# Performance work log

Hardware: AMD Instinct MI355X
Metric: run time of the kernel (lower is better)

The kernel has to match this reference:

```python
import jax, jax.numpy as jnp
import numpy as np

B, N, E, H = 16, 577, 1024, 16          # batch, tokens (1 cls + 24x24 patches), embed, heads
HD = E // H
LORA_E, LORA_R = 4, 16                   # LoRA experts, rank
AD_E, AD_D = 4, 64                       # adapter experts, bottleneck
FF = 4 * E


def setup_inputs() -> dict:
    key = jax.random.key(0)
    ks = jax.random.split(key, 12)
    p = lambda i, shape: jax.random.normal(ks[i], shape, dtype=jnp.float32) * 0.02
    return {
        "tokens": jax.random.normal(ks[0], (B, N, E), dtype=jnp.float32),
        "ln1_g": jnp.ones((E,), jnp.float32), "ln1_b": jnp.zeros((E,), jnp.float32),
        "qkv_w": p(1, (3 * E, E)), "qkv_b": jnp.zeros((3 * E,), jnp.float32),
        "proj_w": p(2, (E, E)), "proj_b": jnp.zeros((E,), jnp.float32),
        "lora_gate_w": p(3, (LORA_E, E)),
        "lora_A": p(4, (LORA_E, LORA_R, E)),
        "lora_B": p(5, (LORA_E, 3 * E, LORA_R)),
        "ln2_g": jnp.ones((E,), jnp.float32), "ln2_b": jnp.zeros((E,), jnp.float32),
        "fc1_w": p(6, (FF, E)), "fc1_b": jnp.zeros((FF,), jnp.float32),
        "fc2_w": p(7, (E, FF)), "fc2_b": jnp.zeros((E,), jnp.float32),
        "ad_gate_w": p(8, (AD_E, E)),
        "ad_down_w": p(9, (AD_E, AD_D, E)), "ad_down_b": jnp.zeros((AD_E, AD_D), jnp.float32),
        "ad_up_w": p(10, (AD_E, E, AD_D)), "ad_up_b": jnp.zeros((AD_E, E), jnp.float32),
    }


def _ln(x, g, b):
    m = x.mean(-1, keepdims=True)
    v = ((x - m) ** 2).mean(-1, keepdims=True)
    return (x - m) * jax.lax.rsqrt(v + 1e-6) * g + b


def reference(tokens, ln1_g, ln1_b, qkv_w, qkv_b, proj_w, proj_b,
              lora_gate_w, lora_A, lora_B, ln2_g, ln2_b,
              fc1_w, fc1_b, fc2_w, fc2_b,
              ad_gate_w, ad_down_w, ad_down_b, ad_up_w, ad_up_b):
    # ---- attention with MoE-LoRA delta on fused QKV ----
    normed = _ln(tokens, ln1_g, ln1_b)                      # [B,N,E]
    qkv = normed @ qkv_w.T + qkv_b                          # [B,N,3E]
    gates = jax.nn.softmax(normed @ lora_gate_w.T, axis=-1)  # [B,N,X]
    h = jnp.einsum('bnd,xrd->bnxr', normed, lora_A)         # low-rank down
    delta = jnp.einsum('bnxr,bnx,xor->bno', h, gates, lora_B)  # gate-weighted up
    qkv = (qkv + delta).reshape(B, N, 3, H, HD).transpose(2, 0, 3, 1, 4)
    q, k, v = qkv[0], qkv[1], qkv[2]                        # [B,H,N,hd]
    scores = jnp.einsum('bhqd,bhkd->bhqk', q, k) * (HD ** -0.5)
    probs = jax.nn.softmax(scores, axis=-1)
    ctx = jnp.einsum('bhqk,bhkd->bhqd', probs, v)
    ctx = ctx.transpose(0, 2, 1, 3).reshape(B, N, E)
    tokens = tokens + (ctx @ proj_w.T + proj_b)
    # ---- MLP + MoE adapter branch (shared norm2 input) ----
    mlp_in = _ln(tokens, ln2_g, ln2_b)
    mlp_out = jax.nn.gelu(mlp_in @ fc1_w.T + fc1_b, approximate=False) @ fc2_w.T + fc2_b
    ag = jax.nn.softmax(mlp_in @ ad_gate_w.T, axis=-1)       # [B,N,Xa]
    ah = jax.nn.gelu(jnp.einsum('bnd,xhd->bnxh', mlp_in, ad_down_w) + ad_down_b,
                     approximate=False)
    ad_out = (jnp.einsum('bnxh,bnx,xoh->bno', ah, ag, ad_up_w)
              + jnp.einsum('bnx,xo->bno', ag, ad_up_b))
    return tokens + mlp_out + ad_out
```

## Files before the change

### kernel.cpp

```cpp
#include <hip/hip_runtime.h>
#include <math.h>

#define TOK 9232
#define EMB 1024
#define NQKV 3072
#define FFD 4096
#define NSEQ 577

typedef __bf16 bf16x8 __attribute__((ext_vector_type(8)));
typedef float f32x4 __attribute__((ext_vector_type(4)));
typedef unsigned short ushort8 __attribute__((ext_vector_type(8)));
typedef unsigned short ushort4v __attribute__((ext_vector_type(4)));

typedef __attribute__((address_space(3))) unsigned int lds_u32_t;
typedef const __attribute__((address_space(1))) unsigned int glob_u32_t;

__device__ __forceinline__ void async16(void* lds, const void* g) {
    __builtin_amdgcn_global_load_lds((glob_u32_t*)g, (lds_u32_t*)lds, 16, 0, 0);
}

__device__ __forceinline__ unsigned short f2bf(float f) {
    unsigned int u = __builtin_bit_cast(unsigned int, f);
    u = (u + 0x7fffu + ((u >> 16) & 1u)) >> 16;
    return (unsigned short)u;
}
__device__ __forceinline__ float bf2f(unsigned short s) {
    unsigned int u = ((unsigned int)s) << 16;
    return __builtin_bit_cast(float, u);
}
__device__ __forceinline__ float gelu_exact(float x) {
    return 0.5f * x * (1.0f + erff(x * 0.70710678118654752f));
}

__global__ void k_pack_all(const float* __restrict__ s_qkv, const float* __restrict__ s_proj,
                           const float* __restrict__ s_fc1, const float* __restrict__ s_fc2,
                           const float* __restrict__ s_la,  const float* __restrict__ s_ad,
                           unsigned short* __restrict__ d_qkv, unsigned short* __restrict__ d_proj,
                           unsigned short* __restrict__ d_fc1, unsigned short* __restrict__ d_fc2,
                           unsigned short* __restrict__ d_la,  unsigned short* __restrict__ d_ad) {
    int stride = gridDim.x * 256;
    for (int i4 = blockIdx.x * 256 + threadIdx.x; i4 < 3227648; i4 += stride) {
        const float* s; unsigned short* d; int local;
        if (i4 < 786432)       { s = s_qkv;  d = d_qkv;  local = i4; }
        else if (i4 < 1048576) { s = s_proj; d = d_proj; local = i4 - 786432; }
        else if (i4 < 2097152) { s = s_fc1;  d = d_fc1;  local = i4 - 1048576; }
        else if (i4 < 3145728) { s = s_fc2;  d = d_fc2;  local = i4 - 2097152; }
        else if (i4 < 3162112) { s = s_la;   d = d_la;   local = i4 - 3145728; }
        else                   { s = s_ad;   d = d_ad;   local = i4 - 3162112; }
        float4 v = ((const float4*)s)[local];
        ushort4v o;
        o[0] = f2bf(v.x); o[1] = f2bf(v.y); o[2] = f2bf(v.z); o[3] = f2bf(v.w);
        ((ushort4v*)d)[local] = o;
    }
}
__global__ void k_pack_bcat(const float* __restrict__ Bw, unsigned short* __restrict__ out) {
    int i = blockIdx.x * 256 + threadIdx.x;
    if (i >= 3072 * 64) return;
    int o = i >> 6, j = i & 63, x = j >> 4, r = j & 15;
    out[o * 64 + j] = f2bf(Bw[x * 3072 * 16 + o * 16 + r]);
}
__global__ void k_pack_u(const float* __restrict__ Uw, unsigned short* __restrict__ out) {
    int i = blockIdx.x * 256 + threadIdx.x;
    if (i >= 1024 * 256) return;
    int o = i >> 8, j = i & 255, x = j >> 6, h = j & 63;
    out[o * 256 + j] = f2bf(Uw[x * 65536 + o * 64 + h]);
}

__global__ __launch_bounds__(256) void k_ln_gates(const float* __restrict__ x,
                                                  const float* __restrict__ g,
                                                  const float* __restrict__ b,
                                                  const float* __restrict__ gw,
                                                  unsigned short* __restrict__ out,
                                                  float* __restrict__ gates) {
    int t = blockIdx.x;
    int tid = threadIdx.x;
    const float* xp = x + (size_t)t * EMB;
    float4 v = ((const float4*)xp)[tid];
    float s = v.x + v.y + v.z + v.w;
    float sq = v.x * v.x + v.y * v.y + v.z * v.z + v.w * v.w;
    #pragma unroll
    for (int off = 32; off > 0; off >>= 1) {
        s += __shfl_down(s, off);
        sq += __shfl_down(sq, off);
    }
    __shared__ float red[8];
    if ((tid & 63) == 0) { red[tid >> 6] = s; red[(tid >> 6) + 4] = sq; }
    __syncthreads();
    float S = red[0] + red[1] + red[2] + red[3];
    float SQ = red[4] + red[5] + red[6] + red[7];
    float mean = S * (1.0f / EMB);
    float var = SQ * (1.0f / EMB) - mean * mean;
    float rstd = rsqrtf(var + 1e-6f);
    float4 gv = ((const float4*)g)[tid];
    float4 bv = ((const float4*)b)[tid];
    float n0 = (v.x - mean) * rstd * gv.x + bv.x;
    float n1 = (v.y - mean) * rstd * gv.y + bv.y;
    float n2 = (v.z - mean) * rstd * gv.z + bv.z;
    float n3 = (v.w - mean) * rstd * gv.w + bv.w;
    ushort4v o;
    o[0] = f2bf(n0); o[1] = f2bf(n1); o[2] = f2bf(n2); o[3] = f2bf(n3);
    ((ushort4v*)(out + (size_t)t * EMB))[tid] = o;
    float p[4];
    #pragma unroll
    for (int xx = 0; xx < 4; ++xx) {
        float4 gr = ((const float4*)(gw + xx * EMB))[tid];
        p[xx] = n0 * gr.x + n1 * gr.y + n2 * gr.z + n3 * gr.w;
    }
    #pragma unroll
    for (int off = 32; off > 0; off >>= 1) {
        #pragma unroll
        for (int xx = 0; xx < 4; ++xx) p[xx] += __shfl_down(p[xx], off);
    }
    __shared__ float red2[4][4];
    if ((tid & 63) == 0) {
        #pragma unroll
        for (int xx = 0; xx < 4; ++xx) red2[tid >> 6][xx] = p[xx];
    }
    __syncthreads();
    if (tid == 0) {
        float l[4];
        #pragma unroll
        for (int xx = 0; xx < 4; ++xx) l[xx] = red2[0][xx] + red2[1][xx] + red2[2][xx] + red2[3][xx];
        float m = fmaxf(fmaxf(l[0], l[1]), fmaxf(l[2], l[3]));
        float e[4], ssum = 0.f;
        #pragma unroll
        for (int xx = 0; xx < 4; ++xx) { e[xx] = expf(l[xx] - m); ssum += e[xx]; }
        float inv = 1.0f / ssum;
        #pragma unroll
        for (int xx = 0; xx < 4; ++xx) gates[t * 4 + xx] = e[xx] * inv;
    }
}

__global__ __launch_bounds__(256) void k_fc2init(const float* __restrict__ tok2,
                                                 const float* __restrict__ fc2b,
                                                 const float* __restrict__ ag,
                                                 const float* __restrict__ upb,
                                                 float* __restrict__ out) {
    int t = blockIdx.x;
    int tid = threadIdx.x;
    float g0 = ag[t * 4 + 0], g1 = ag[t * 4 + 1], g2 = ag[t * 4 + 2], g3 = ag[t * 4 + 3];
    float4 b0 = ((const float4*)(upb + 0 * EMB))[tid];
    float4 b1 = ((const float4*)(upb + 1 * EMB))[tid];
    float4 b2 = ((const float4*)(upb + 2 * EMB))[tid];
    float4 b3 = ((const float4*)(upb + 3 * EMB))[tid];
    float4 fb = ((const float4*)fc2b)[tid];
    float4 r = ((const float4*)(tok2 + (size_t)t * EMB))[tid];
    r.x += fb.x + g0 * b0.x + g1 * b1.x + g2 * b2.x + g3 * b3.x;
    r.y += fb.y + g0 * b0.y + g1 * b1.y + g2 * b2.y + g3 * b3.y;
    r.z += fb.z + g0 * b0.z + g1 * b1.z + g2 * b2.z + g3 * b3.z;
    r.w += fb.w + g0 * b0.w + g1 * b1.w + g2 * b2.w + g3 * b3.w;
    ((float4*)(out + (size_t)t * EMB))[tid] = r;
}

#define BAR __builtin_amdgcn_s_barrier()

template<bool GELU, bool BF16OUT, int GG, int MF>
__global__ __launch_bounds__(256) void k_gemm(
    const unsigned short* __restrict__ A, int lda,
    const unsigned short* __restrict__ W, int ldw, int K1,
    int M, int N,
    const unsigned short* __restrict__ A2, const unsigned short* __restrict__ W2, int K2,
    const float* __restrict__ bias, const float* __restrict__ resid,
    const float* __restrict__ aux,
    void* __restrict__ Cout, int ldc, int gy)
{
    constexpr int CA = MF * 2;
    constexpr int CPW = (CA + 8) / 4;
    constexpr int BUFB = (CA + 8) * 1024;
    __shared__ __attribute__((aligned(16))) char Sbuf[3 * BUFB];

    int tid = threadIdx.x;
    int nwg = gridDim.x, orig = blockIdx.x;
    int xcd = orig & 7, lid = orig >> 3;
    int q = nwg >> 3, r = nwg & 7;
    int wg = (xcd < r ? xcd * (q + 1) : r * (q + 1) + (xcd - r) * q) + lid;
    int bm = (wg / gy) * (MF * 32);
    int bn = (wg % gy) * 128;

    int l = tid & 63, w = tid >> 6;
    int wr = w >> 1, wc = w & 1;
    int lr = l & 15;
    int sslot = (((l & 3) ^ ((l >> 3) & 3)) << 3);

    int KT1 = K1 >> 5, KT2 = K2 >> 5;
    int KT = KT1 + KT2;

    const unsigned short* A2s = A2 ? A2 : A;
    const unsigned short* W2s = W2 ? W2 : W;
    int K2s = A2 ? K2 : lda;

    const unsigned short* sp1[CPW];
    const unsigned short* sp2[CPW];
    int ldsu[CPW];
    #pragma unroll
    for (int j = 0; j < CPW; ++j) {
        int c = w * CPW + j;
        ldsu[j] = c << 10;
        if (c < CA) {
            int rw = bm + c * 16 + (l >> 2); if (rw > M - 1) rw = M - 1;
            sp1[j] = A + (size_t)rw * lda + sslot;
            sp2[j] = A2s + (size_t)rw * K2s + sslot;
        } else {
            int rw = bn + (c - CA) * 16 + (l >> 2); if (rw > N - 1) rw = N - 1;
            sp1[j] = W + (size_t)rw * ldw + sslot;
            sp2[j] = W2s + (size_t)rw * K2s + sslot;
        }
    }

    int psl = ((l >> 4) ^ ((lr >> 1) & 3)) << 4;
    int offA[MF], offB[4];
    #pragma unroll
    for (int m = 0; m < MF; ++m) offA[m] = ((wr * (MF * 16) + m * 16 + lr) << 6) + psl;
    #pragma unroll
    for (int n = 0; n < 4; ++n) offB[n] = (CA << 10) + ((wc * 64 + n * 16 + lr) << 6) + psl;

    f32x4 acc[MF][4];
    #pragma unroll
    for (int m = 0; m < MF; ++m)
        #pragma unroll
        for (int n = 0; n < 4; ++n) acc[m][n] = (f32x4){0.f, 0.f, 0.f, 0.f};

    auto stage = [&](int ss, int sb_) {
        char* db = Sbuf + sb_ * BUFB;
        if (ss < KT1) {
            int ko = ss << 5;
            #pragma unroll
            for (int j = 0; j < CPW; ++j) async16(db + ldsu[j], sp1[j] + ko);
        } else {
            int ko = (ss - KT1) << 5;
            #pragma unroll
            for (int j = 0; j < CPW; ++j) async16(db + ldsu[j], sp2[j] + ko);
        }
    };

    stage(0, 0);
    stage(1, 1);

    int cb = 0, sb = 2;
    #pragma unroll 1
    for (int t = 0; t < KT; ++t) {
        if constexpr (CPW == 4) asm volatile("s_waitcnt vmcnt(4)" ::: "memory");
        else                    asm volatile("s_waitcnt vmcnt(3)" ::: "memory");
        BAR;
        __builtin_amdgcn_sched_barrier(0);
        int s = t + 2; if (s >= KT) s = 0;
        stage(s, sb);
        const char* base = Sbuf + cb * BUFB;
        bf16x8 af[MF], bfr[4];
        #pragma unroll
        for (int m = 0; m < MF; ++m) af[m] = *(const bf16x8*)(base + offA[m]);
        #pragma unroll
        for (int n = 0; n < 4; ++n) bfr[n] = *(const bf16x8*)(base + offB[n]);
        __builtin_amdgcn_s_setprio(1);
        #pragma unroll
        for (int m = 0; m < MF; ++m)
            #pragma unroll
            for (int n = 0; n < 4; ++n)
                acc[m][n] = __builtin_amdgcn_mfma_f32_16x16x32_bf16(af[m], bfr[n], acc[m][n], 0, 0, 0);
        __builtin_amdgcn_s_setprio(0);
        cb = (cb == 2) ? 0 : cb + 1;
        sb = (sb == 2) ? 0 : sb + 1;
    }

    int rbase = bm + wr * (MF * 16);
    int cbase = bn + wc * 64;
    #pragma unroll
    for (int n = 0; n < 4; ++n) {
        int col = cbase + n * 16 + lr;
        if (col >= N) continue;
        float bv = bias ? bias[col] : 0.0f;
        #pragma unroll
        for (int m = 0; m < MF; ++m) {
            #pragma unroll
            for (int rr = 0; rr < 4; ++rr) {
                int row = rbase + m * 16 + (l >> 4) * 4 + rr;
                if (row >= M) continue;
                float c = acc[m][n][rr] + bv;
                if (GELU) c = gelu_exact(c);
                if (GG > 0) c *= aux[row * 4 + col / (GG > 0 ? GG : 1)];
                if (resid) c += resid[(size_t)row * ldc + col];
                if (BF16OUT) ((unsigned short*)Cout)[(size_t)row * ldc + col] = f2bf(c);
                else ((float*)Cout)[(size_t)row * ldc + col] = c;
            }
        }
    }
}

__global__ __launch_bounds__(256) void k_attn(const unsigned short* __restrict__ qkv,
                                              unsigned short* __restrict__ ctx) {
    int bh = blockIdx.x;
    int qt = blockIdx.y;
    int b = bh >> 4, h = bh & 15;
    int tid = threadIdx.x;
    int l = tid & 63;
    int w = tid >> 6;
    int lr = l & 15;
    int lk = (l >> 4) * 8;

    __shared__ unsigned short Qs[64][72];
    __shared__ unsigned short Ks[64][72];
    __shared__ unsigned short Vt[64][72];
    __shared__ unsigned short Ps[64][72];

    const size_t base = (size_t)b * NSEQ * NQKV + (size_t)h * 64;
    int q0 = qt * 64;

    {
        int row = tid >> 2, ds = (tid & 3) * 16;
        int qrow = q0 + row;
        if (qrow < NSEQ) {
            const unsigned short* src = qkv + base + (size_t)qrow * NQKV + ds;
            #pragma unroll
            for (int j = 0; j < 16; ++j) Qs[row][ds + j] = f2bf(bf2f(src[j]) * 0.125f);
        } else {
            #pragma unroll
            for (int j = 0; j < 16; ++j) Qs[row][ds + j] = 0;
        }
    }

    float m_run[4], l_run[4];
    f32x4 o[4];
    #pragma unroll
    for (int r = 0; r < 4; ++r) { m_run[r] = -1e30f; l_run[r] = 0.0f; }
    #pragma unroll
    for (int n = 0; n < 4; ++n) o[n] = (f32x4){0.f, 0.f, 0.f, 0.f};

    for (int kt = 0; kt < 10; ++kt) {
        __syncthreads();
        {
            int row = tid >> 2, ds = (tid & 3) * 16;
            int key = kt * 64 + row;
            if (key < NSEQ) {
                const unsigned short* ksrc = qkv + base + (size_t)key * NQKV + 1024 + ds;
                *(ushort8*)&Ks[row][ds] = *(const ushort8*)ksrc;
                *(ushort8*)&Ks[row][ds + 8] = *(const ushort8*)(ksrc + 8);
                const unsigned short* vsrc = qkv + base + (size_t)key * NQKV + 2048 + ds;
                #pragma unroll
                for (int j = 0; j < 16; ++j) Vt[ds + j][row] = vsrc[j];
            } else {
                ushort8 z = {};
                *(ushort8*)&Ks[row][ds] = z;
                *(ushort8*)&Ks[row][ds + 8] = z;
                #pragma unroll
                for (int j = 0; j < 16; ++j) Vt[ds + j][row] = 0;
            }
        }
        __syncthreads();

        f32x4 s[4];
        #pragma unroll
        for (int n = 0; n < 4; ++n) s[n] = (f32x4){0.f, 0.f, 0.f, 0.f};
        #pragma unroll
        for (int ks = 0; ks < 2; ++ks) {
            bf16x8 qa = *(const bf16x8*)&Qs[w * 16 + lr][ks * 32 + lk];
            #pragma unroll
            for (int n = 0; n < 4; ++n) {
                bf16x8 kb = *(const bf16x8*)&Ks[n * 16 + lr][ks * 32 + lk];
                s[n] = __builtin_amdgcn_mfma_f32_16x16x32_bf16(qa, kb, s[n], 0, 0, 0);
            }
        }
        #pragma unroll
        for (int n = 0; n < 4; ++n) {
            int col = kt * 64 + n * 16 + lr;
            if (col >= NSEQ) {
                #pragma unroll
                for (int r = 0; r < 4; ++r) s[n][r] = -1e30f;
            }
        }
        float tmax[4];
        #pragma unroll
        for (int r = 0; r < 4; ++r)
            tmax[r] = fmaxf(fmaxf(s[0][r], s[1][r]), fmaxf(s[2][r], s[3][r]));
        #pragma unroll
        for (int off = 1; off < 16; off <<= 1) {
            #pragma unroll
            for (int r = 0; r < 4; ++r) tmax[r] = fmaxf(tmax[r], __shfl_xor(tmax[r], off));
        }
        float alpha[4], rs[4];
        #pragma unroll
        for (int r = 0; r < 4; ++r) {
            float mn = fmaxf(m_run[r], tmax[r]);
            alpha[r] = __expf(m_run[r] - mn);
            m_run[r] = mn;
            rs[r] = 0.0f;
        }
        #pragma unroll
        for (int n = 0; n < 4; ++n) {
            #pragma unroll
            for (int r = 0; r < 4; ++r) {
                float p = __expf(s[n][r] - m_run[r]);
                s[n][r] = p;
                rs[r] += p;
            }
        }
        #pragma unroll
        for (int off = 1; off < 16; off <<= 1) {
            #pragma unroll
            for (int r = 0; r < 4; ++r) rs[r] += __shfl_xor(rs[r], off);
        }
        #pragma unroll
        for (int r = 0; r < 4; ++r) l_run[r] = l_run[r] * alpha[r] + rs[r];
        #pragma unroll
        for (int n = 0; n < 4; ++n) {
            #pragma unroll
            for (int r = 0; r < 4; ++r) o[n][r] *= alpha[r];
        }
        #pragma unroll
        for (int n = 0; n < 4; ++n) {
            #pragma unroll
            for (int r = 0; r < 4; ++r)
                Ps[w * 16 + (l >> 4) * 4 + r][n * 16 + lr] = f2bf(s[n][r]);
        }
        __syncthreads();
        #pragma unroll
        for (int ks = 0; ks < 2; ++ks) {
            bf16x8 pa = *(const bf16x8*)&Ps[w * 16 + lr][ks * 32 + lk];
            #pragma unroll
            for (int n = 0; n < 4; ++n) {
                bf16x8 vb = *(const bf16x8*)&Vt[n * 16 + lr][ks * 32 + lk];
                o[n] = __builtin_amdgcn_mfma_f32_16x16x32_bf16(pa, vb, o[n], 0, 0, 0);
            }
        }
    }
    #pragma unroll
    for (int r = 0; r < 4; ++r) {
        int qrow = q0 + w * 16 + (l >> 4) * 4 + r;
        if (qrow < NSEQ) {
            float inv = (l_run[r] > 0.f) ? 1.0f / l_run[r] : 0.0f;
            #pragma unroll
            for (int n = 0; n < 4; ++n)
                ctx[((size_t)b * NSEQ + qrow) * EMB + h * 64 + n * 16 + lr] = f2bf(o[n][r] * inv);
        }
    }
}

extern "C" void kernel_launch(void* const* d_in, const int* in_sizes, int n_in,
                              void* d_out, int out_size, void* d_ws, size_t ws_size,
                              hipStream_t stream) {
    const float* tokens      = (const float*)d_in[0];
    const float* ln1_g       = (const float*)d_in[1];
    const float* ln1_b       = (const float*)d_in[2];
    const float* qkv_w       = (const float*)d_in[3];
    const float* qkv_b       = (const float*)d_in[4];
    const float* proj_w      = (const float*)d_in[5];
    const float* proj_b      = (const float*)d_in[6];
    const float* lora_gate_w = (const float*)d_in[7];
    const float* lora_A      = (const float*)d_in[8];
    const float* lora_B      = (const float*)d_in[9];
    const float* ln2_g       = (const float*)d_in[10];
    const float* ln2_b       = (const float*)d_in[11];
    const float* fc1_w       = (const float*)d_in[12];
    const float* fc1_b       = (const float*)d_in[13];
    const float* fc2_w       = (const float*)d_in[14];
    const float* fc2_b       = (const float*)d_in[15];
    const float* ad_gate_w   = (const float*)d_in[16];
    const float* ad_down_w   = (const float*)d_in[17];
    const float* ad_down_b   = (const float*)d_in[18];
    const float* ad_up_w     = (const float*)d_in[19];
    const float* ad_up_b     = (const float*)d_in[20];

    char* ws = (char*)d_ws;
    size_t off = 0;
    auto alloc = [&](size_t bytes) -> void* {
        void* p = ws + off;
        off += (bytes + 255) & ~(size_t)255;
        return p;
    };

    unsigned short* w_qkv  = (unsigned short*)alloc((size_t)NQKV * EMB * 2);
    unsigned short* w_proj = (unsigned short*)alloc((size_t)EMB * EMB * 2);
    unsigned short* w_fc1  = (unsigned short*)alloc((size_t)FFD * EMB * 2);
    unsigned short* w_fc2  = (unsigned short*)alloc((size_t)EMB * FFD * 2);
    unsigned short* w_acat = (unsigned short*)alloc((size_t)64 * EMB * 2);
    unsigned short* w_bcat = (unsigned short*)alloc((size_t)NQKV * 64 * 2);
    unsigned short* w_dcat = (unsigned short*)alloc((size_t)256 * EMB * 2);
    unsigned short* w_u    = (unsigned short*)alloc((size_t)EMB * 256 * 2);

    unsigned short* u1 = (unsigned short*)alloc((size_t)TOK * EMB * 2);
    unsigned short* u2 = (unsigned short*)alloc((size_t)TOK * EMB * 2);
    unsigned short* u3 = (unsigned short*)alloc((size_t)TOK * FFD * 2);
    float* tok2  = (float*)alloc((size_t)TOK * EMB * 4);
    unsigned short* hw  = (unsigned short*)alloc((size_t)TOK * 64 * 2);
    unsigned short* ahw = (unsigned short*)alloc((size_t)TOK * 256 * 2);
    float* gates = (float*)alloc((size_t)TOK * 4 * 4);
    float* ag    = (float*)alloc((size_t)TOK * 4 * 4);

    unsigned short* normed = u1;
    unsigned short* mlpin  = u1;
    unsigned short* ctx    = u2;
    unsigned short* qkv    = u3;
    unsigned short* h1     = u3;

    k_pack_all<<<2048, 256, 0, stream>>>(qkv_w, proj_w, fc1_w, fc2_w, lora_A, ad_down_w,
                                         w_qkv, w_proj, w_fc1, w_fc2, w_acat, w_dcat);
    k_pack_bcat<<<(NQKV * 64 + 255) / 256, 256, 0, stream>>>(lora_B, w_bcat);
    k_pack_u<<<(EMB * 256 + 255) / 256, 256, 0, stream>>>(ad_up_w, w_u);

    k_ln_gates<<<TOK, 256, 0, stream>>>(tokens, ln1_g, ln1_b, lora_gate_w, normed, gates);
    k_gemm<false, true, 16, 2><<<145, 256, 0, stream>>>(
        normed, EMB, w_acat, EMB, EMB, TOK, 64,
        nullptr, nullptr, 0, nullptr, nullptr, gates, hw, 64, 1);
    k_gemm<false, true, 0, 4><<<73 * 24, 256, 0, stream>>>(
        normed, EMB, w_qkv, EMB, EMB, TOK, NQKV,
        hw, w_bcat, 64, qkv_b, nullptr, nullptr, qkv, NQKV, 24);
    k_attn<<<dim3(256, 10), 256, 0, stream>>>(qkv, ctx);
    k_gemm<false, false, 0, 2><<<145 * 8, 256, 0, stream>>>(
        ctx, EMB, w_proj, EMB, EMB, TOK, EMB,
        nullptr, nullptr, 0, proj_b, tokens, nullptr, tok2, EMB, 8);
    k_ln_gates<<<TOK, 256, 0, stream>>>(tok2, ln2_g, ln2_b, ad_gate_w, mlpin, ag);
    k_gemm<true, true, 64, 2><<<145 * 2, 256, 0, stream>>>(
        mlpin, EMB, w_dcat, EMB, EMB, TOK, 256,
        nullptr, nullptr, 0, ad_down_b, nullptr, ag, ahw, 256, 2);
    k_fc2init<<<TOK, 256, 0, stream>>>(tok2, fc2_b, ag, ad_up_b, (float*)d_out);
    k_gemm<true, true, 0, 4><<<73 * 32, 256, 0, stream>>>(
        mlpin, EMB, w_fc1, EMB, EMB, TOK, FFD,
        nullptr, nullptr, 0, fc1_b, nullptr, nullptr, h1, FFD, 32);
    k_gemm<false, false, 0, 2><<<145 * 8, 256, 0, stream>>>(
        h1, FFD, w_fc2, FFD, FFD, TOK, EMB,
        ahw, w_u, 256, nullptr, (const float*)d_out, nullptr, (float*)d_out, EMB, 8);
}
```

Before: 721.6 us.

## Double K-tile depth to 64 with 2-stage buffering in GEMM kernel

The bf16 MFMA GEMM now loads K-tiles of 64 instead of 32, using a 128-byte row layout with an 8-way XOR swizzle. Pipelining drops from triple buffering to double buffering. The goal is to halve the number of barriers and loop iterations per K and to issue more MFMAs per sync point. In exchange, each stage waits on vmcnt(0), so less load latency is hidden. LDS use per block also grows, which may lower occupancy.

```diff
diff --git a/kernel.cpp b/kernel.cpp
--- a/kernel.cpp
+++ b/kernel.cpp
@@ -164,10 +164,11 @@
     const float* __restrict__ aux,
     void* __restrict__ Cout, int ldc, int gy)
 {
-    constexpr int CA = MF * 2;
-    constexpr int CPW = (CA + 8) / 4;
-    constexpr int BUFB = (CA + 8) * 1024;
-    __shared__ __attribute__((aligned(16))) char Sbuf[3 * BUFB];
+    constexpr int CA = MF * 4;
+    constexpr int CT = CA + 16;
+    constexpr int CPW = CT / 4;
+    constexpr int BUFB = CT * 1024;
+    __shared__ __attribute__((aligned(16))) char Sbuf[2 * BUFB];
 
     int tid = threadIdx.x;
     int nwg = gridDim.x, orig = blockIdx.x;
@@ -180,9 +181,9 @@
     int l = tid & 63, w = tid >> 6;
     int wr = w >> 1, wc = w & 1;
     int lr = l & 15;
-    int sslot = (((l & 3) ^ ((l >> 3) & 3)) << 3);
-
-    int KT1 = K1 >> 5, KT2 = K2 >> 5;
+    int sslot = (((l & 7) ^ (l >> 3)) << 3);
+
+    int KT1 = K1 >> 6, KT2 = K2 >> 6;
     int KT = KT1 + KT2;
 
     const unsigned short* A2s = A2 ? A2 : A;
@@ -197,22 +198,33 @@
         int c = w * CPW + j;
         ldsu[j] = c << 10;
         if (c < CA) {
-            int rw = bm + c * 16 + (l >> 2); if (rw > M - 1) rw = M - 1;
+            int rw = bm + c * 8 + (l >> 3); if (rw > M - 1) rw = M - 1;
             sp1[j] = A + (size_t)rw * lda + sslot;
             sp2[j] = A2s + (size_t)rw * K2s + sslot;
         } else {
-            int rw = bn + (c - CA) * 16 + (l >> 2); if (rw > N - 1) rw = N - 1;
+            int rw = bn + (c - CA) * 8 + (l >> 3); if (rw > N - 1) rw = N - 1;
             sp1[j] = W + (size_t)rw * ldw + sslot;
             sp2[j] = W2s + (size_t)rw * K2s + sslot;
         }
     }
 
-    int psl = ((l >> 4) ^ ((lr >> 1) & 3)) << 4;
-    int offA[MF], offB[4];
-    #pragma unroll
-    for (int m = 0; m < MF; ++m) offA[m] = ((wr * (MF * 16) + m * 16 + lr) << 6) + psl;
-    #pragma unroll
-    for (int n = 0; n < 4; ++n) offB[n] = (CA << 10) + ((wc * 64 + n * 16 + lr) << 6) + psl;
+    int offA[MF][2], offB[4][2];
+    #pragma unroll
+    for (int m = 0; m < MF; ++m)
+        #pragma unroll
+        for (int ks = 0; ks < 2; ++ks) {
+            int rw = wr * (MF * 16) + m * 16 + lr;
+            int g = ks * 4 + (l >> 4);
+            offA[m][ks] = (rw << 7) + ((g ^ (rw & 7)) << 4);
+        }
+    #pragma unroll
+    for (int n = 0; n < 4; ++n)
+        #pragma unroll
+        for (int ks = 0; ks < 2; ++ks) {
+            int rw = wc * 64 + n * 16 + lr;
+            int g = ks * 4 + (l >> 4);
+            offB[n][ks] = (CA << 10) + (rw << 7) + ((g ^ (rw & 7)) << 4);
+        }
 
     f32x4 acc[MF][4];
     #pragma unroll
@@ -220,46 +232,47 @@
         #pragma unroll
         for (int n = 0; n < 4; ++n) acc[m][n] = (f32x4){0.f, 0.f, 0.f, 0.f};
 
-    auto stage = [&](int ss, int sb_) {
-        char* db = Sbuf + sb_ * BUFB;
+    auto stage = [&](int ss, int bb) {
+        char* db = Sbuf + bb * BUFB;
         if (ss < KT1) {
-            int ko = ss << 5;
+            int ko = ss << 6;
             #pragma unroll
             for (int j = 0; j < CPW; ++j) async16(db + ldsu[j], sp1[j] + ko);
         } else {
-            int ko = (ss - KT1) << 5;
+            int ko = (ss - KT1) << 6;
             #pragma unroll
             for (int j = 0; j < CPW; ++j) async16(db + ldsu[j], sp2[j] + ko);
         }
     };
 
     stage(0, 0);
-    stage(1, 1);
-
-    int cb = 0, sb = 2;
+
     #pragma unroll 1
     for (int t = 0; t < KT; ++t) {
-        if constexpr (CPW == 4) asm volatile("s_waitcnt vmcnt(4)" ::: "memory");
-        else                    asm volatile("s_waitcnt vmcnt(3)" ::: "memory");
+        asm volatile("s_waitcnt vmcnt(0)" ::: "memory");
         BAR;
         __builtin_amdgcn_sched_barrier(0);
-        int s = t + 2; if (s >= KT) s = 0;
-        stage(s, sb);
-        const char* base = Sbuf + cb * BUFB;
-        bf16x8 af[MF], bfr[4];
-        #pragma unroll
-        for (int m = 0; m < MF; ++m) af[m] = *(const bf16x8*)(base + offA[m]);
-        #pragma unroll
-        for (int n = 0; n < 4; ++n) bfr[n] = *(const bf16x8*)(base + offB[n]);
+        int s = t + 1; if (s >= KT) s = 0;
+        stage(s, (t + 1) & 1);
+        const char* base = Sbuf + (t & 1) * BUFB;
+        bf16x8 af[MF][2], bfr[4][2];
+        #pragma unroll
+        for (int m = 0; m < MF; ++m)
+            #pragma unroll
+            for (int ks = 0; ks < 2; ++ks) af[m][ks] = *(const bf16x8*)(base + offA[m][ks]);
+        #pragma unroll
+        for (int n = 0; n < 4; ++n)
+            #pragma unroll
+            for (int ks = 0; ks < 2; ++ks) bfr[n][ks] = *(const bf16x8*)(base + offB[n][ks]);
         __builtin_amdgcn_s_setprio(1);
         #pragma unroll
         for (int m = 0; m < MF; ++m)
             #pragma unroll
             for (int n = 0; n < 4; ++n)
-                acc[m][n] = __builtin_amdgcn_mfma_f32_16x16x32_bf16(af[m], bfr[n], acc[m][n], 0, 0, 0);
+                #pragma unroll
+                for (int ks = 0; ks < 2; ++ks)
+                    acc[m][n] = __builtin_amdgcn_mfma_f32_16x16x32_bf16(af[m][ks], bfr[n][ks], acc[m][n], 0, 0, 0);
         __builtin_amdgcn_s_setprio(0);
-        cb = (cb == 2) ? 0 : cb + 1;
-        sb = (sb == 2) ? 0 : sb + 1;
     }
 
     int rbase = bm + wr * (MF * 16);
```

New measurement: 721.9 us. Within noise of the previous version (+0.0%).
